# Kernel optimization log

Hardware: AMD Instinct MI355X
Metric: run time of the kernel (lower is better)

## Reference

```python
import jax, jax.numpy as jnp
import numpy as np

N, HID, H, D = 2048, 1024, 16, 64


def setup_inputs() -> dict:
    key = jax.random.key(0)
    ks = jax.random.split(key, 10)
    s_in = 1.0 / np.sqrt(HID)      # Linear(hidden -> H*D) init scale
    s_o = 1.0 / np.sqrt(H * D)     # Linear(H*D -> D) init scale
    return {
        "x": jax.random.normal(ks[0], (N, HID), jnp.float32),
        "history": jnp.zeros((H, N, N), jnp.float32),
        "Wq_w": jax.random.uniform(ks[1], (H * D, HID), jnp.float32, -s_in, s_in),
        "Wq_b": jax.random.uniform(ks[2], (H * D,), jnp.float32, -s_in, s_in),
        "Wk_w": jax.random.uniform(ks[3], (H * D, HID), jnp.float32, -s_in, s_in),
        "Wk_b": jax.random.uniform(ks[4], (H * D,), jnp.float32, -s_in, s_in),
        "Wv_w": jax.random.uniform(ks[5], (H * D, HID), jnp.float32, -s_in, s_in),
        "Wv_b": jax.random.uniform(ks[6], (H * D,), jnp.float32, -s_in, s_in),
        "Wo_w": jax.random.uniform(ks[7], (D, H * D), jnp.float32, -s_o, s_o),
        "Wo_b": jax.random.uniform(ks[8], (D,), jnp.float32, -s_o, s_o),
        "beta": jnp.float32(0.1),
    }


def reference(x, history, Wq_w, Wq_b, Wk_w, Wk_b, Wv_w, Wv_b, Wo_w, Wo_b, beta):
    n = x.shape[0]
    # QKV projections: [N, H*D] -> [H, N, D]
    q = (x @ Wq_w.T + Wq_b).reshape(n, H, D).transpose(1, 0, 2)
    k = (x @ Wk_w.T + Wk_b).reshape(n, H, D).transpose(1, 0, 2)
    v = (x @ Wv_w.T + Wv_b).reshape(n, H, D).transpose(1, 0, 2)
    scores = jnp.einsum('hnd,hmd->hnm', q, k) / np.sqrt(D).astype(np.float32)
    scores = scores + beta * history  # learned additive history bias
    attn = jax.nn.softmax(scores, axis=-1)  # [H, N, N]
    new_history = history + jax.lax.stop_gradient(attn)  # stateful accumulation (detached)
    out = jnp.einsum('hnm,hmd->hnd', attn, v)  # [H, N, D]
    out = out.transpose(1, 0, 2).reshape(n, H * D)
    out = out @ Wo_w.T + Wo_b  # [N, D]
    # dropout is identity (p=0.0 / eval)
    return (out, attn, new_history)
```

## Files before the change

kernel.cpp:

```cpp
#include <hip/hip_runtime.h>
#include <hip/hip_bf16.h>

#define N_TOK 2048
#define HIDDEN 1024
#define NHEAD 16
#define DHEAD 64

typedef __attribute__((ext_vector_type(8))) short bf16x8;
typedef __attribute__((ext_vector_type(4))) float f32x4;

__device__ inline unsigned short f2bf(float x) {
    __hip_bfloat16 h = __float2bfloat16(x);
    return *reinterpret_cast<unsigned short*>(&h);
}

__device__ inline f32x4 zero4() {
    f32x4 z;
    z[0] = 0.f; z[1] = 0.f; z[2] = 0.f; z[3] = 0.f;
    return z;
}

__global__ void cvt4_kernel(const float* __restrict__ x, const float* __restrict__ wq,
                            const float* __restrict__ wk, const float* __restrict__ wv,
                            unsigned short* __restrict__ dst) {
    int i = blockIdx.x * blockDim.x + threadIdx.x;
    const float* src;
    int off;
    if (i < 524288)       { src = x;  off = i; }
    else if (i < 786432)  { src = wq; off = i - 524288; }
    else if (i < 1048576) { src = wk; off = i - 786432; }
    else                  { src = wv; off = i - 1048576; }
    float4 v = reinterpret_cast<const float4*>(src)[off];
    ushort4 o;
    o.x = f2bf(v.x); o.y = f2bf(v.y); o.z = f2bf(v.z); o.w = f2bf(v.w);
    reinterpret_cast<ushort4*>(dst)[i] = o;
}

__launch_bounds__(256)
__global__ void gemm_qkv(const unsigned short* __restrict__ xb,
                         const unsigned short* __restrict__ wb,
                         const float* __restrict__ bq, const float* __restrict__ bk,
                         const float* __restrict__ bv,
                         unsigned short* __restrict__ qb, unsigned short* __restrict__ kb,
                         unsigned short* __restrict__ vb) {
    __shared__ unsigned short As[2][128 * 64];
    __shared__ unsigned short Bs[2][128 * 64];
    const int tid = threadIdx.x;
    const int lane = tid & 63;
    const int w = tid >> 6;
    const int wr = w >> 1, wc = w & 1;
    const int rb = blockIdx.y * 128;
    const int cb = blockIdx.x * 128;
    const int r0 = tid >> 3, c0 = tid & 7;

    f32x4 acc[4][4];
    for (int i = 0; i < 4; i++)
        for (int j = 0; j < 4; j++) acc[i][j] = zero4();

    uint4 va[4], vb4[4];
#pragma unroll
    for (int i = 0; i < 4; i++) {
        va[i]  = *reinterpret_cast<const uint4*>(xb + (size_t)(rb + r0 + 32 * i) * HIDDEN + c0 * 8);
        vb4[i] = *reinterpret_cast<const uint4*>(wb + (size_t)(cb + r0 + 32 * i) * HIDDEN + c0 * 8);
    }
#pragma unroll
    for (int i = 0; i < 4; i++) {
        int row = r0 + 32 * i;
        *reinterpret_cast<uint4*>(As[0] + row * 64 + ((c0 ^ (row & 7)) << 3)) = va[i];
        *reinterpret_cast<uint4*>(Bs[0] + row * 64 + ((c0 ^ (row & 7)) << 3)) = vb4[i];
    }
    __syncthreads();
    int cur = 0;

    for (int kt = 0; kt < 16; ++kt) {
        if (kt < 15) {
#pragma unroll
            for (int i = 0; i < 4; i++) {
                va[i]  = *reinterpret_cast<const uint4*>(xb + (size_t)(rb + r0 + 32 * i) * HIDDEN + (kt + 1) * 64 + c0 * 8);
                vb4[i] = *reinterpret_cast<const uint4*>(wb + (size_t)(cb + r0 + 32 * i) * HIDDEN + (kt + 1) * 64 + c0 * 8);
            }
        }
#pragma unroll
        for (int kk = 0; kk < 2; kk++) {
            bf16x8 a[4], b[4];
#pragma unroll
            for (int mi = 0; mi < 4; mi++) {
                int row = wr * 64 + mi * 16 + (lane & 15);
                a[mi] = *reinterpret_cast<const bf16x8*>(As[cur] + row * 64 + (((kk * 4 + (lane >> 4)) ^ (row & 7)) << 3));
            }
#pragma unroll
            for (int ni = 0; ni < 4; ni++) {
                int row = wc * 64 + ni * 16 + (lane & 15);
                b[ni] = *reinterpret_cast<const bf16x8*>(Bs[cur] + row * 64 + (((kk * 4 + (lane >> 4)) ^ (row & 7)) << 3));
            }
#pragma unroll
            for (int mi = 0; mi < 4; mi++)
#pragma unroll
                for (int ni = 0; ni < 4; ni++)
                    acc[mi][ni] = __builtin_amdgcn_mfma_f32_16x16x32_bf16(a[mi], b[ni], acc[mi][ni], 0, 0, 0);
        }
        if (kt < 15) {
#pragma unroll
            for (int i = 0; i < 4; i++) {
                int row = r0 + 32 * i;
                *reinterpret_cast<uint4*>(As[cur ^ 1] + row * 64 + ((c0 ^ (row & 7)) << 3)) = va[i];
                *reinterpret_cast<uint4*>(Bs[cur ^ 1] + row * 64 + ((c0 ^ (row & 7)) << 3)) = vb4[i];
            }
        }
        __syncthreads();
        cur ^= 1;
    }

    const int region = blockIdx.x >> 3;
    const float* bias = region == 0 ? bq : (region == 1 ? bk : bv);
    unsigned short* dst = region == 0 ? qb : (region == 1 ? kb : vb);
#pragma unroll
    for (int mi = 0; mi < 4; mi++) {
#pragma unroll
        for (int ni = 0; ni < 4; ni++) {
            int colg = cb + wc * 64 + ni * 16 + (lane & 15);
            int jj = colg & 1023;
            int hh = jj >> 6, d = jj & 63;
            float bval = bias[jj];
#pragma unroll
            for (int r = 0; r < 4; r++) {
                int n = rb + wr * 64 + mi * 16 + ((lane >> 4) << 2) + r;
                dst[((size_t)hh * N_TOK + n) * 64 + d] = f2bf(acc[mi][ni][r] + bval);
            }
        }
    }
}

__global__ void transpose_v(const unsigned short* __restrict__ vb, unsigned short* __restrict__ vbt) {
    int t = blockIdx.x * blockDim.x + threadIdx.x;
    int nc = t & 255, d = (t >> 8) & 63, h = t >> 14;
    int n0 = nc * 8;
    unsigned short tmp[8];
#pragma unroll
    for (int j = 0; j < 8; j++)
        tmp[j] = vb[((size_t)h * N_TOK + n0 + j) * 64 + d];
    *reinterpret_cast<uint4*>(vbt + ((size_t)h * 64 + d) * N_TOK + n0) = *reinterpret_cast<uint4*>(tmp);
}

__launch_bounds__(256)
__global__ void attn_stats(const unsigned short* __restrict__ qb,
                           const unsigned short* __restrict__ kb,
                           const float* __restrict__ hist,
                           const float* __restrict__ beta_p,
                           float* __restrict__ m_part,
                           float* __restrict__ l_part) {
    __shared__ unsigned short Ks[2][64 * 64];
    const int tid = threadIdx.x;
    const int lane = tid & 63;
    const int g = lane >> 4;
    const int q15 = lane & 15;
    const int w = tid >> 6;
    const int chunk = blockIdx.x;
    const int rb = blockIdx.y;
    const int h = blockIdx.z;
    const int n0 = rb * 64;
    const int c_base = chunk * 512;
    const float beta = beta_p[0];
    const float scale = 0.125f;
    const int qrow = w * 16 + q15;

    const unsigned short* qsrc = qb + ((size_t)h * N_TOK + n0 + qrow) * 64;
    bf16x8 aq0 = *reinterpret_cast<const bf16x8*>(qsrc + 8 * g);
    bf16x8 aq1 = *reinterpret_cast<const bf16x8*>(qsrc + 8 * g + 32);

    const int jr = tid >> 3, jc = tid & 7;

    float m = -1e30f, l = 0.0f;
    const float* hbase = hist + ((size_t)h * N_TOK + n0 + qrow) * N_TOK + c_base + 4 * g;

    f32x4 h4[4], h4n[4];
    {
        uint4 k0 = *reinterpret_cast<const uint4*>(kb + ((size_t)h * N_TOK + c_base + jr) * 64 + jc * 8);
        uint4 k1 = *reinterpret_cast<const uint4*>(kb + ((size_t)h * N_TOK + c_base + jr + 32) * 64 + jc * 8);
#pragma unroll
        for (int nt = 0; nt < 4; nt++) h4[nt] = *reinterpret_cast<const f32x4*>(hbase + nt * 16);
        *reinterpret_cast<uint4*>(Ks[0] + jr * 64 + ((jc ^ (jr & 7)) << 3)) = k0;
        *reinterpret_cast<uint4*>(Ks[0] + (jr + 32) * 64 + ((jc ^ ((jr + 32) & 7)) << 3)) = k1;
    }
    __syncthreads();
    int cur = 0;

    for (int t = 0; t < 8; t++) {
        uint4 k0, k1;
        if (t < 7) {
            k0 = *reinterpret_cast<const uint4*>(kb + ((size_t)h * N_TOK + c_base + (t + 1) * 64 + jr) * 64 + jc * 8);
            k1 = *reinterpret_cast<const uint4*>(kb + ((size_t)h * N_TOK + c_base + (t + 1) * 64 + jr + 32) * 64 + jc * 8);
#pragma unroll
            for (int nt = 0; nt < 4; nt++)
                h4n[nt] = *reinterpret_cast<const f32x4*>(hbase + (t + 1) * 64 + nt * 16);
        }

        f32x4 s_acc[4];
#pragma unroll
        for (int nt = 0; nt < 4; nt++) {
            s_acc[nt] = zero4();
            int krow = nt * 16 + q15;
            bf16x8 kf0 = *reinterpret_cast<const bf16x8*>(Ks[cur] + krow * 64 + ((g ^ (q15 & 7)) << 3));
            bf16x8 kf1 = *reinterpret_cast<const bf16x8*>(Ks[cur] + krow * 64 + (((4 + g) ^ (q15 & 7)) << 3));
            s_acc[nt] = __builtin_amdgcn_mfma_f32_16x16x32_bf16(kf0, aq0, s_acc[nt], 0, 0, 0);
            s_acc[nt] = __builtin_amdgcn_mfma_f32_16x16x32_bf16(kf1, aq1, s_acc[nt], 0, 0, 0);
        }
        float sc[4][4];
#pragma unroll
        for (int nt = 0; nt < 4; nt++)
#pragma unroll
            for (int r = 0; r < 4; r++)
                sc[nt][r] = s_acc[nt][r] * scale + beta * h4[nt][r];

        float tm = sc[0][0];
#pragma unroll
        for (int nt = 0; nt < 4; nt++)
#pragma unroll
            for (int r = 0; r < 4; r++) tm = fmaxf(tm, sc[nt][r]);
        tm = fmaxf(tm, __shfl_xor(tm, 16));
        tm = fmaxf(tm, __shfl_xor(tm, 32));
        float mn = fmaxf(m, tm);
        float ps = 0.0f;
#pragma unroll
        for (int nt = 0; nt < 4; nt++)
#pragma unroll
            for (int r = 0; r < 4; r++) ps += __expf(sc[nt][r] - mn);
        ps += __shfl_xor(ps, 16);
        ps += __shfl_xor(ps, 32);
        l = l * __expf(m - mn) + ps;
        m = mn;

        if (t < 7) {
            *reinterpret_cast<uint4*>(Ks[cur ^ 1] + jr * 64 + ((jc ^ (jr & 7)) << 3)) = k0;
            *reinterpret_cast<uint4*>(Ks[cur ^ 1] + (jr + 32) * 64 + ((jc ^ ((jr + 32) & 7)) << 3)) = k1;
#pragma unroll
            for (int nt = 0; nt < 4; nt++) h4[nt] = h4n[nt];
        }
        __syncthreads();
        cur ^= 1;
    }

    if (lane < 16) {
        const int base = ((h * 32 + rb) * 4 + chunk) * 64;
        m_part[base + w * 16 + lane] = m;
        l_part[base + w * 16 + lane] = l;
    }
}

__launch_bounds__(256)
__global__ void attn_finalize(const unsigned short* __restrict__ qb,
                              const unsigned short* __restrict__ kb,
                              const unsigned short* __restrict__ vbt,
                              const float* __restrict__ hist,
                              const float* __restrict__ beta_p,
                              const float* __restrict__ m_part,
                              const float* __restrict__ l_part,
                              float* __restrict__ attn_out,
                              float* __restrict__ nh_out,
                              float* __restrict__ opart) {
    __shared__ unsigned short Ks[2][64 * 64];
    __shared__ unsigned short Vs[2][64 * 64];
    __shared__ unsigned short Ps[4][16 * 64];
    const int tid = threadIdx.x;
    const int lane = tid & 63;
    const int g = lane >> 4;
    const int q15 = lane & 15;
    const int w = tid >> 6;
    const int chunk = blockIdx.x;
    const int rb = blockIdx.y;
    const int h = blockIdx.z;
    const int n0 = rb * 64;
    const int c_base = chunk * 512;
    const float beta = beta_p[0];
    const float scale = 0.125f;
    const int qrow = w * 16 + q15;

    const unsigned short* qsrc = qb + ((size_t)h * N_TOK + n0 + qrow) * 64;
    bf16x8 aq0 = *reinterpret_cast<const bf16x8*>(qsrc + 8 * g);
    bf16x8 aq1 = *reinterpret_cast<const bf16x8*>(qsrc + 8 * g + 32);

    float m_row, inv_l;
    {
        const int pbase = (h * 32 + rb) * 4 * 64;
        float m0 = m_part[pbase + 0 * 64 + qrow];
        float m1 = m_part[pbase + 1 * 64 + qrow];
        float m2 = m_part[pbase + 2 * 64 + qrow];
        float m3 = m_part[pbase + 3 * 64 + qrow];
        float mm = fmaxf(fmaxf(m0, m1), fmaxf(m2, m3));
        float ll = l_part[pbase + 0 * 64 + qrow] * __expf(m0 - mm)
                 + l_part[pbase + 1 * 64 + qrow] * __expf(m1 - mm)
                 + l_part[pbase + 2 * 64 + qrow] * __expf(m2 - mm)
                 + l_part[pbase + 3 * 64 + qrow] * __expf(m3 - mm);
        m_row = mm;
        inv_l = 1.0f / ll;
    }

    f32x4 oacc[4];
#pragma unroll
    for (int di = 0; di < 4; di++) oacc[di] = zero4();

    const int jr = tid >> 3, jc = tid & 7;
    unsigned short* Psw = Ps[w];
    const float* hbase = hist + ((size_t)h * N_TOK + n0 + qrow) * N_TOK + c_base + 4 * g;
    float* abase = attn_out + ((size_t)h * N_TOK + n0 + qrow) * N_TOK + c_base + 4 * g;
    float* nbase = nh_out + ((size_t)h * N_TOK + n0 + qrow) * N_TOK + c_base + 4 * g;

    f32x4 h4[4], h4n[4];
    {
        uint4 k0 = *reinterpret_cast<const uint4*>(kb + ((size_t)h * N_TOK + c_base + jr) * 64 + jc * 8);
        uint4 k1 = *reinterpret_cast<const uint4*>(kb + ((size_t)h * N_TOK + c_base + jr + 32) * 64 + jc * 8);
        uint4 v0 = *reinterpret_cast<const uint4*>(vbt + ((size_t)h * 64 + jr) * N_TOK + c_base + jc * 8);
        uint4 v1 = *reinterpret_cast<const uint4*>(vbt + ((size_t)h * 64 + jr + 32) * N_TOK + c_base + jc * 8);
#pragma unroll
        for (int nt = 0; nt < 4; nt++) h4[nt] = *reinterpret_cast<const f32x4*>(hbase + nt * 16);
        *reinterpret_cast<uint4*>(Ks[0] + jr * 64 + ((jc ^ (jr & 7)) << 3)) = k0;
        *reinterpret_cast<uint4*>(Ks[0] + (jr + 32) * 64 + ((jc ^ ((jr + 32) & 7)) << 3)) = k1;
        *reinterpret_cast<uint4*>(Vs[0] + jr * 64 + ((jc ^ (jr & 7)) << 3)) = v0;
        *reinterpret_cast<uint4*>(Vs[0] + (jr + 32) * 64 + ((jc ^ ((jr + 32) & 7)) << 3)) = v1;
    }
    __syncthreads();
    int cur = 0;

    for (int t = 0; t < 8; t++) {
        uint4 k0, k1, v0, v1;
        if (t < 7) {
            const int c1 = c_base + (t + 1) * 64;
            k0 = *reinterpret_cast<const uint4*>(kb + ((size_t)h * N_TOK + c1 + jr) * 64 + jc * 8);
            k1 = *reinterpret_cast<const uint4*>(kb + ((size_t)h * N_TOK + c1 + jr + 32) * 64 + jc * 8);
            v0 = *reinterpret_cast<const uint4*>(vbt + ((size_t)h * 64 + jr) * N_TOK + c1 + jc * 8);
            v1 = *reinterpret_cast<const uint4*>(vbt + ((size_t)h * 64 + jr + 32) * N_TOK + c1 + jc * 8);
#pragma unroll
            for (int nt = 0; nt < 4; nt++)
                h4n[nt] = *reinterpret_cast<const f32x4*>(hbase + (t + 1) * 64 + nt * 16);
        }

        f32x4 s_acc[4];
#pragma unroll
        for (int nt = 0; nt < 4; nt++) {
            s_acc[nt] = zero4();
            int krow = nt * 16 + q15;
            bf16x8 kf0 = *reinterpret_cast<const bf16x8*>(Ks[cur] + krow * 64 + ((g ^ (q15 & 7)) << 3));
            bf16x8 kf1 = *reinterpret_cast<const bf16x8*>(Ks[cur] + krow * 64 + (((4 + g) ^ (q15 & 7)) << 3));
            s_acc[nt] = __builtin_amdgcn_mfma_f32_16x16x32_bf16(kf0, aq0, s_acc[nt], 0, 0, 0);
            s_acc[nt] = __builtin_amdgcn_mfma_f32_16x16x32_bf16(kf1, aq1, s_acc[nt], 0, 0, 0);
        }

#pragma unroll
        for (int nt = 0; nt < 4; nt++) {
            float a0 = __expf(s_acc[nt][0] * scale + beta * h4[nt][0] - m_row) * inv_l;
            float a1 = __expf(s_acc[nt][1] * scale + beta * h4[nt][1] - m_row) * inv_l;
            float a2 = __expf(s_acc[nt][2] * scale + beta * h4[nt][2] - m_row) * inv_l;
            float a3 = __expf(s_acc[nt][3] * scale + beta * h4[nt][3] - m_row) * inv_l;
            f32x4 av, nv;
            av[0] = a0; av[1] = a1; av[2] = a2; av[3] = a3;
            nv[0] = a0 + h4[nt][0]; nv[1] = a1 + h4[nt][1];
            nv[2] = a2 + h4[nt][2]; nv[3] = a3 + h4[nt][3];
            *reinterpret_cast<f32x4*>(abase + t * 64 + nt * 16) = av;
            *reinterpret_cast<f32x4*>(nbase + t * 64 + nt * 16) = nv;
            ushort4 p;
            p.x = f2bf(a0); p.y = f2bf(a1); p.z = f2bf(a2); p.w = f2bf(a3);
            *reinterpret_cast<ushort4*>(Psw + q15 * 64 + (((4 * nt + g) ^ (q15 & 14)) << 2)) = p;
        }

#pragma unroll
        for (int kk2 = 0; kk2 < 2; kk2++) {
            bf16x8 pa = *reinterpret_cast<const bf16x8*>(Psw + q15 * 64 + (((8 * kk2 + 2 * g) ^ (q15 & 14)) << 2));
#pragma unroll
            for (int di = 0; di < 4; di++) {
                int vrow = di * 16 + q15;
                bf16x8 vf = *reinterpret_cast<const bf16x8*>(Vs[cur] + vrow * 64 + (((kk2 * 4 + g) ^ (q15 & 7)) << 3));
                oacc[di] = __builtin_amdgcn_mfma_f32_16x16x32_bf16(pa, vf, oacc[di], 0, 0, 0);
            }
        }

        if (t < 7) {
            *reinterpret_cast<uint4*>(Ks[cur ^ 1] + jr * 64 + ((jc ^ (jr & 7)) << 3)) = k0;
            *reinterpret_cast<uint4*>(Ks[cur ^ 1] + (jr + 32) * 64 + ((jc ^ ((jr + 32) & 7)) << 3)) = k1;
            *reinterpret_cast<uint4*>(Vs[cur ^ 1] + jr * 64 + ((jc ^ (jr & 7)) << 3)) = v0;
            *reinterpret_cast<uint4*>(Vs[cur ^ 1] + (jr + 32) * 64 + ((jc ^ ((jr + 32) & 7)) << 3)) = v1;
#pragma unroll
            for (int nt = 0; nt < 4; nt++) h4[nt] = h4n[nt];
        }
        __syncthreads();
        cur ^= 1;
    }

#pragma unroll
    for (int di = 0; di < 4; di++) {
#pragma unroll
        for (int r = 0; r < 4; r++) {
            int rl = w * 16 + g * 4 + r;
            int d = di * 16 + q15;
            opart[((size_t)(chunk * NHEAD + h) * N_TOK + n0 + rl) * 64 + d] = oacc[di][r];
        }
    }
}

__global__ void reduce_hv(const float4* __restrict__ op, float4* __restrict__ hv) {
    size_t i = (size_t)blockIdx.x * blockDim.x + threadIdx.x;
    const size_t C = (size_t)NHEAD * N_TOK * DHEAD / 4;
    float4 a = op[i], b = op[i + C], c = op[i + 2 * C], d = op[i + 3 * C];
    float4 r;
    r.x = a.x + b.x + c.x + d.x;
    r.y = a.y + b.y + c.y + d.y;
    r.z = a.z + b.z + c.z + d.z;
    r.w = a.w + b.w + c.w + d.w;
    hv[i] = r;
}

__launch_bounds__(256)
__global__ void out_proj(const float* __restrict__ hv, const float* __restrict__ Wo,
                         const float* __restrict__ bo, float* __restrict__ out) {
    __shared__ float wos[64][129];
    const int tid = threadIdx.x;
    const int dd = tid & 63;
    const int w = tid >> 6;
    const int n0 = blockIdx.x * 16;
    float acc[4] = {0.f, 0.f, 0.f, 0.f};
    for (int kc = 0; kc < 1024; kc += 128) {
        __syncthreads();
#pragma unroll
        for (int i = 0; i < 32; i++) {
            int e = tid + 256 * i;
            int r = e >> 7, j = e & 127;
            wos[r][j] = Wo[(size_t)r * 1024 + kc + j];
        }
        __syncthreads();
#pragma unroll 4
        for (int k = 0; k < 128; k++) {
            float wv = wos[dd][k];
            int jg = kc + k;
            const float* hb = hv + ((size_t)(jg >> 6) * N_TOK) * 64 + (jg & 63);
#pragma unroll
            for (int q = 0; q < 4; q++) {
                acc[q] += hb[(size_t)(n0 + w + 4 * q) * 64] * wv;
            }
        }
    }
#pragma unroll
    for (int q = 0; q < 4; q++)
        out[(size_t)(n0 + w + 4 * q) * 64 + dd] = acc[q] + bo[dd];
}

extern "C" void kernel_launch(void* const* d_in, const int* in_sizes, int n_in,
                              void* d_out, int out_size, void* d_ws, size_t ws_size,
                              hipStream_t stream) {
    const float* x    = (const float*)d_in[0];
    const float* hist = (const float*)d_in[1];
    const float* Wq_w = (const float*)d_in[2];
    const float* Wq_b = (const float*)d_in[3];
    const float* Wk_w = (const float*)d_in[4];
    const float* Wk_b = (const float*)d_in[5];
    const float* Wv_w = (const float*)d_in[6];
    const float* Wv_b = (const float*)d_in[7];
    const float* Wo_w = (const float*)d_in[8];
    const float* Wo_b = (const float*)d_in[9];
    const float* beta = (const float*)d_in[10];

    float* out = (float*)d_out;
    float* attn_out = out + 131072;
    float* nh_out = attn_out + (size_t)NHEAD * N_TOK * N_TOK;

    unsigned short* xb  = (unsigned short*)d_ws;
    unsigned short* wb  = xb + (size_t)N_TOK * HIDDEN;
    unsigned short* qb  = wb + (size_t)3 * HIDDEN * HIDDEN;
    unsigned short* kb  = qb + (size_t)N_TOK * HIDDEN;
    unsigned short* vb  = kb + (size_t)N_TOK * HIDDEN;
    unsigned short* vbt = vb + (size_t)N_TOK * HIDDEN;
    float* hvb    = (float*)(vbt + (size_t)N_TOK * HIDDEN);
    float* m_part = hvb + (size_t)N_TOK * HIDDEN;
    float* l_part = m_part + 16 * 32 * 4 * 64;
    float* opart  = l_part + 16 * 32 * 4 * 64;

    cvt4_kernel<<<5120, 256, 0, stream>>>(x, Wq_w, Wk_w, Wv_w, xb);
    gemm_qkv<<<dim3(24, 16), 256, 0, stream>>>(xb, wb, Wq_b, Wk_b, Wv_b, qb, kb, vb);
    transpose_v<<<1024, 256, 0, stream>>>(vb, vbt);
    attn_stats<<<dim3(4, 32, 16), 256, 0, stream>>>(qb, kb, hist, beta, m_part, l_part);
    attn_finalize<<<dim3(4, 32, 16), 256, 0, stream>>>(qb, kb, vbt, hist, beta, m_part, l_part,
                                                       attn_out, nh_out, opart);
    reduce_hv<<<2048, 256, 0, stream>>>((const float4*)opart, (float4*)hvb);
    out_proj<<<128, 256, 0, stream>>>(hvb, Wo_w, Wo_b, out);
}
```

Before: 461.5 us.

## Load K/V MFMA fragments directly from global memory, drop LDS staging and barriers

Both attention kernels stop staging K and V tiles through double-buffered shared memory with __syncthreads. Each wave now reads its MFMA fragments straight from global memory, relying on L1/L2 for reuse across the four waves. The attn and new_history stores become nontemporal to avoid polluting cache. This trades barrier and LDS traffic for redundant global/L2 loads and loses the explicit software prefetch of history and K/V.

After: 611.5 us. +32.5%, slower.

```diff
diff --git a/kernel.cpp b/kernel.cpp
--- a/kernel.cpp
+++ b/kernel.cpp
@@ -149,7 +149,6 @@
                            const float* __restrict__ beta_p,
                            float* __restrict__ m_part,
                            float* __restrict__ l_part) {
-    __shared__ unsigned short Ks[2][64 * 64];
     const int tid = threadIdx.x;
     const int lane = tid & 63;
     const int g = lane >> 4;
@@ -168,41 +167,24 @@
     bf16x8 aq0 = *reinterpret_cast<const bf16x8*>(qsrc + 8 * g);
     bf16x8 aq1 = *reinterpret_cast<const bf16x8*>(qsrc + 8 * g + 32);
 
-    const int jr = tid >> 3, jc = tid & 7;
+    const unsigned short* kfb = kb + ((size_t)h * N_TOK + c_base + q15) * 64 + 8 * g;
 
     float m = -1e30f, l = 0.0f;
     const float* hbase = hist + ((size_t)h * N_TOK + n0 + qrow) * N_TOK + c_base + 4 * g;
 
-    f32x4 h4[4], h4n[4];
-    {
-        uint4 k0 = *reinterpret_cast<const uint4*>(kb + ((size_t)h * N_TOK + c_base + jr) * 64 + jc * 8);
-        uint4 k1 = *reinterpret_cast<const uint4*>(kb + ((size_t)h * N_TOK + c_base + jr + 32) * 64 + jc * 8);
-#pragma unroll
-        for (int nt = 0; nt < 4; nt++) h4[nt] = *reinterpret_cast<const f32x4*>(hbase + nt * 16);
-        *reinterpret_cast<uint4*>(Ks[0] + jr * 64 + ((jc ^ (jr & 7)) << 3)) = k0;
-        *reinterpret_cast<uint4*>(Ks[0] + (jr + 32) * 64 + ((jc ^ ((jr + 32) & 7)) << 3)) = k1;
-    }
-    __syncthreads();
-    int cur = 0;
-
     for (int t = 0; t < 8; t++) {
-        uint4 k0, k1;
-        if (t < 7) {
-            k0 = *reinterpret_cast<const uint4*>(kb + ((size_t)h * N_TOK + c_base + (t + 1) * 64 + jr) * 64 + jc * 8);
-            k1 = *reinterpret_cast<const uint4*>(kb + ((size_t)h * N_TOK + c_base + (t + 1) * 64 + jr + 32) * 64 + jc * 8);
-#pragma unroll
-            for (int nt = 0; nt < 4; nt++)
-                h4n[nt] = *reinterpret_cast<const f32x4*>(hbase + (t + 1) * 64 + nt * 16);
-        }
+        f32x4 h4[4];
+#pragma unroll
+        for (int nt = 0; nt < 4; nt++)
+            h4[nt] = *reinterpret_cast<const f32x4*>(hbase + t * 64 + nt * 16);
 
         f32x4 s_acc[4];
 #pragma unroll
         for (int nt = 0; nt < 4; nt++) {
-            s_acc[nt] = zero4();
-            int krow = nt * 16 + q15;
-            bf16x8 kf0 = *reinterpret_cast<const bf16x8*>(Ks[cur] + krow * 64 + ((g ^ (q15 & 7)) << 3));
-            bf16x8 kf1 = *reinterpret_cast<const bf16x8*>(Ks[cur] + krow * 64 + (((4 + g) ^ (q15 & 7)) << 3));
-            s_acc[nt] = __builtin_amdgcn_mfma_f32_16x16x32_bf16(kf0, aq0, s_acc[nt], 0, 0, 0);
+            const unsigned short* kr = kfb + (size_t)(t * 64 + nt * 16) * 64;
+            bf16x8 kf0 = *reinterpret_cast<const bf16x8*>(kr);
+            bf16x8 kf1 = *reinterpret_cast<const bf16x8*>(kr + 32);
+            s_acc[nt] = __builtin_amdgcn_mfma_f32_16x16x32_bf16(kf0, aq0, zero4(), 0, 0, 0);
             s_acc[nt] = __builtin_amdgcn_mfma_f32_16x16x32_bf16(kf1, aq1, s_acc[nt], 0, 0, 0);
         }
         float sc[4][4];
@@ -229,15 +211,6 @@
         ps += __shfl_xor(ps, 32);
         l = l * __expf(m - mn) + ps;
         m = mn;
-
-        if (t < 7) {
-            *reinterpret_cast<uint4*>(Ks[cur ^ 1] + jr * 64 + ((jc ^ (jr & 7)) << 3)) = k0;
-            *reinterpret_cast<uint4*>(Ks[cur ^ 1] + (jr + 32) * 64 + ((jc ^ ((jr + 32) & 7)) << 3)) = k1;
-#pragma unroll
-            for (int nt = 0; nt < 4; nt++) h4[nt] = h4n[nt];
-        }
-        __syncthreads();
-        cur ^= 1;
     }
 
     if (lane < 16) {
@@ -258,8 +231,6 @@
                               float* __restrict__ attn_out,
                               float* __restrict__ nh_out,
                               float* __restrict__ opart) {
-    __shared__ unsigned short Ks[2][64 * 64];
-    __shared__ unsigned short Vs[2][64 * 64];
     __shared__ unsigned short Ps[4][16 * 64];
     const int tid = threadIdx.x;
     const int lane = tid & 63;
@@ -299,49 +270,26 @@
 #pragma unroll
     for (int di = 0; di < 4; di++) oacc[di] = zero4();
 
-    const int jr = tid >> 3, jc = tid & 7;
     unsigned short* Psw = Ps[w];
+    const unsigned short* kfb = kb + ((size_t)h * N_TOK + c_base + q15) * 64 + 8 * g;
+    const unsigned short* vfb = vbt + ((size_t)h * 64 + q15) * N_TOK + c_base + 8 * g;
     const float* hbase = hist + ((size_t)h * N_TOK + n0 + qrow) * N_TOK + c_base + 4 * g;
     float* abase = attn_out + ((size_t)h * N_TOK + n0 + qrow) * N_TOK + c_base + 4 * g;
     float* nbase = nh_out + ((size_t)h * N_TOK + n0 + qrow) * N_TOK + c_base + 4 * g;
 
-    f32x4 h4[4], h4n[4];
-    {
-        uint4 k0 = *reinterpret_cast<const uint4*>(kb + ((size_t)h * N_TOK + c_base + jr) * 64 + jc * 8);
-        uint4 k1 = *reinterpret_cast<const uint4*>(kb + ((size_t)h * N_TOK + c_base + jr + 32) * 64 + jc * 8);
-        uint4 v0 = *reinterpret_cast<const uint4*>(vbt + ((size_t)h * 64 + jr) * N_TOK + c_base + jc * 8);
-        uint4 v1 = *reinterpret_cast<const uint4*>(vbt + ((size_t)h * 64 + jr + 32) * N_TOK + c_base + jc * 8);
-#pragma unroll
-        for (int nt = 0; nt < 4; nt++) h4[nt] = *reinterpret_cast<const f32x4*>(hbase + nt * 16);
-        *reinterpret_cast<uint4*>(Ks[0] + jr * 64 + ((jc ^ (jr & 7)) << 3)) = k0;
-        *reinterpret_cast<uint4*>(Ks[0] + (jr + 32) * 64 + ((jc ^ ((jr + 32) & 7)) << 3)) = k1;
-        *reinterpret_cast<uint4*>(Vs[0] + jr * 64 + ((jc ^ (jr & 7)) << 3)) = v0;
-        *reinterpret_cast<uint4*>(Vs[0] + (jr + 32) * 64 + ((jc ^ ((jr + 32) & 7)) << 3)) = v1;
-    }
-    __syncthreads();
-    int cur = 0;
-
     for (int t = 0; t < 8; t++) {
-        uint4 k0, k1, v0, v1;
-        if (t < 7) {
-            const int c1 = c_base + (t + 1) * 64;
-            k0 = *reinterpret_cast<const uint4*>(kb + ((size_t)h * N_TOK + c1 + jr) * 64 + jc * 8);
-            k1 = *reinterpret_cast<const uint4*>(kb + ((size_t)h * N_TOK + c1 + jr + 32) * 64 + jc * 8);
-            v0 = *reinterpret_cast<const uint4*>(vbt + ((size_t)h * 64 + jr) * N_TOK + c1 + jc * 8);
-            v1 = *reinterpret_cast<const uint4*>(vbt + ((size_t)h * 64 + jr + 32) * N_TOK + c1 + jc * 8);
-#pragma unroll
-            for (int nt = 0; nt < 4; nt++)
-                h4n[nt] = *reinterpret_cast<const f32x4*>(hbase + (t + 1) * 64 + nt * 16);
-        }
+        f32x4 h4[4];
+#pragma unroll
+        for (int nt = 0; nt < 4; nt++)
+            h4[nt] = *reinterpret_cast<const f32x4*>(hbase + t * 64 + nt * 16);
 
         f32x4 s_acc[4];
 #pragma unroll
         for (int nt = 0; nt < 4; nt++) {
-            s_acc[nt] = zero4();
-            int krow = nt * 16 + q15;
-            bf16x8 kf0 = *reinterpret_cast<const bf16x8*>(Ks[cur] + krow * 64 + ((g ^ (q15 & 7)) << 3));
-            bf16x8 kf1 = *reinterpret_cast<const bf16x8*>(Ks[cur] + krow * 64 + (((4 + g) ^ (q15 & 7)) << 3));
-            s_acc[nt] = __builtin_amdgcn_mfma_f32_16x16x32_bf16(kf0, aq0, s_acc[nt], 0, 0, 0);
+            const unsigned short* kr = kfb + (size_t)(t * 64 + nt * 16) * 64;
+            bf16x8 kf0 = *reinterpret_cast<const bf16x8*>(kr);
+            bf16x8 kf1 = *reinterpret_cast<const bf16x8*>(kr + 32);
+            s_acc[nt] = __builtin_amdgcn_mfma_f32_16x16x32_bf16(kf0, aq0, zero4(), 0, 0, 0);
             s_acc[nt] = __builtin_amdgcn_mfma_f32_16x16x32_bf16(kf1, aq1, s_acc[nt], 0, 0, 0);
         }
 
@@ -355,8 +303,8 @@
             av[0] = a0; av[1] = a1; av[2] = a2; av[3] = a3;
             nv[0] = a0 + h4[nt][0]; nv[1] = a1 + h4[nt][1];
             nv[2] = a2 + h4[nt][2]; nv[3] = a3 + h4[nt][3];
-            *reinterpret_cast<f32x4*>(abase + t * 64 + nt * 16) = av;
-            *reinterpret_cast<f32x4*>(nbase + t * 64 + nt * 16) = nv;
+            __builtin_nontemporal_store(av, reinterpret_cast<f32x4*>(abase + t * 64 + nt * 16));
+            __builtin_nontemporal_store(nv, reinterpret_cast<f32x4*>(nbase + t * 64 + nt * 16));
             ushort4 p;
             p.x = f2bf(a0); p.y = f2bf(a1); p.z = f2bf(a2); p.w = f2bf(a3);
             *reinterpret_cast<ushort4*>(Psw + q15 * 64 + (((4 * nt + g) ^ (q15 & 14)) << 2)) = p;
@@ -367,22 +315,11 @@
             bf16x8 pa = *reinterpret_cast<const bf16x8*>(Psw + q15 * 64 + (((8 * kk2 + 2 * g) ^ (q15 & 14)) << 2));
 #pragma unroll
             for (int di = 0; di < 4; di++) {
-                int vrow = di * 16 + q15;
-                bf16x8 vf = *reinterpret_cast<const bf16x8*>(Vs[cur] + vrow * 64 + (((kk2 * 4 + g) ^ (q15 & 7)) << 3));
+                const unsigned short* vr = vfb + (size_t)(di * 16) * N_TOK + t * 64 + 32 * kk2;
+                bf16x8 vf = *reinterpret_cast<const bf16x8*>(vr);
                 oacc[di] = __builtin_amdgcn_mfma_f32_16x16x32_bf16(pa, vf, oacc[di], 0, 0, 0);
             }
         }
-
-        if (t < 7) {
-            *reinterpret_cast<uint4*>(Ks[cur ^ 1] + jr * 64 + ((jc ^ (jr & 7)) << 3)) = k0;
-            *reinterpret_cast<uint4*>(Ks[cur ^ 1] + (jr + 32) * 64 + ((jc ^ ((jr + 32) & 7)) << 3)) = k1;
-            *reinterpret_cast<uint4*>(Vs[cur ^ 1] + jr * 64 + ((jc ^ (jr & 7)) << 3)) = v0;
-            *reinterpret_cast<uint4*>(Vs[cur ^ 1] + (jr + 32) * 64 + ((jc ^ ((jr + 32) & 7)) << 3)) = v1;
-#pragma unroll
-            for (int nt = 0; nt < 4; nt++) h4[nt] = h4n[nt];
-        }
-        __syncthreads();
-        cur ^= 1;
     }
 
 #pragma unroll
```
